# Optimization experiments

Measured on AMD Instinct MI355X. Metric: run time of the kernel, lower is better.

## Reference

```python
import jax, jax.numpy as jnp
import numpy as np

LN_EPS = 1e-12  # config.layer_norm_eps (BERT default)


def setup_inputs() -> dict:
    key = jax.random.key(0)
    k1, k2, k3, k4 = jax.random.split(key, 4)
    B, S, D_IN, D_OUT = 16, 512, 4096, 1024
    return {
        "hidden_states": jax.random.normal(k1, (B, S, D_IN), dtype=jnp.float32),
        "input_tensor": jax.random.normal(k2, (B, S, D_OUT), dtype=jnp.float32),
        "W": jax.random.normal(k3, (D_OUT, D_IN), dtype=jnp.float32) * 0.02,
        "b": jax.random.normal(k4, (D_OUT,), dtype=jnp.float32) * 0.02,
        "gamma": jnp.ones((D_OUT,), dtype=jnp.float32),
        "beta": jnp.zeros((D_OUT,), dtype=jnp.float32),
    }


def reference(hidden_states, input_tensor, W, b, gamma, beta):
    # mix_Linear 1-bit path (XNOR-Net style): binarize weights with per-row scale
    alpha = jnp.mean(jnp.abs(W), axis=1, keepdims=True)   # [D_OUT, 1]
    W_q = jnp.sign(W) * alpha                              # [D_OUT, D_IN]
    # dense GEMM: [B,S,D_IN] x [D_OUT,D_IN]^T -> [B,S,D_OUT]
    h = jnp.einsum("bsi,oi->bso", hidden_states, W_q) + b
    # dropout is identity in eval mode; residual add + LayerNorm
    x = h + input_tensor
    mu = jnp.mean(x, axis=-1, keepdims=True)
    var = jnp.mean(jnp.square(x - mu), axis=-1, keepdims=True)
    return gamma * (x - mu) * jax.lax.rsqrt(var + LN_EPS) + beta
```

## Files before the change

### kernel.cpp

```cpp
#include <hip/hip_runtime.h>

using u16    = unsigned short;
using short8 = __attribute__((ext_vector_type(8))) short;
using u16x8  = __attribute__((ext_vector_type(8))) u16;
using u16x4  = __attribute__((ext_vector_type(4))) u16;
using f32x4  = __attribute__((ext_vector_type(4))) float;

#define M_DIM 8192
#define N_DIM 1024
#define K_DIM 4096

typedef __attribute__((address_space(1))) void gvoid;
typedef __attribute__((address_space(3))) void svoid;
#define GLOAD_LDS16(g, s) \
  __builtin_amdgcn_global_load_lds((gvoid*)(void*)(g), (svoid*)(s), 16, 0, 0)

__device__ __forceinline__ u16 f2bf(float f) {
  unsigned u = __builtin_bit_cast(unsigned, f);
  u = (u + 0x7FFFu + ((u >> 16) & 1u)) >> 16;
  return (u16)u;
}

__global__ __launch_bounds__(256) void wprep_kernel(const float* __restrict__ W,
                                                    u16* __restrict__ Wsgn,
                                                    float* __restrict__ alpha) {
  const int row = blockIdx.x;
  const int t   = threadIdx.x;
  const float4* wr = (const float4*)(W + (size_t)row * K_DIM);
  float4 v[4];
  float s = 0.f;
#pragma unroll
  for (int j = 0; j < 4; ++j) {
    v[j] = wr[t + 256 * j];
    s += fabsf(v[j].x) + fabsf(v[j].y) + fabsf(v[j].z) + fabsf(v[j].w);
  }
#pragma unroll
  for (int off = 32; off > 0; off >>= 1) s += __shfl_down(s, off, 64);
  __shared__ float red[4];
  if ((t & 63) == 0) red[t >> 6] = s;
  __syncthreads();
  if (t == 0) alpha[row] = (red[0] + red[1] + red[2] + red[3]) * (1.0f / K_DIM);
  u16x4* dst = (u16x4*)(Wsgn + (size_t)row * K_DIM);
#pragma unroll
  for (int j = 0; j < 4; ++j) {
    u16x4 sg;
    sg[0] = v[j].x > 0.f ? 0x3F80 : (v[j].x < 0.f ? 0xBF80 : 0);
    sg[1] = v[j].y > 0.f ? 0x3F80 : (v[j].y < 0.f ? 0xBF80 : 0);
    sg[2] = v[j].z > 0.f ? 0x3F80 : (v[j].z < 0.f ? 0xBF80 : 0);
    sg[3] = v[j].w > 0.f ? 0x3F80 : (v[j].w < 0.f ? 0xBF80 : 0);
    dst[t + 256 * j] = sg;
  }
}

__global__ __launch_bounds__(256) void cast_kernel(const float* __restrict__ in,
                                                   u16* __restrict__ out) {
  const size_t i = ((size_t)blockIdx.x * 256 + threadIdx.x) * 8;
  float4 a = ((const float4*)(in + i))[0];
  float4 b = ((const float4*)(in + i))[1];
  u16x8 p;
  p[0] = f2bf(a.x); p[1] = f2bf(a.y); p[2] = f2bf(a.z); p[3] = f2bf(a.w);
  p[4] = f2bf(b.x); p[5] = f2bf(b.y); p[6] = f2bf(b.z); p[7] = f2bf(b.w);
  *(u16x8*)(out + i) = p;
}

template <bool PRE>
__global__ __launch_bounds__(256) void gemm_kernel(const void* __restrict__ Aopaque,
                                                   const u16* __restrict__ Bsgn,
                                                   const float* __restrict__ alpha,
                                                   const float* __restrict__ bias,
                                                   const float* __restrict__ resid,
                                                   float* __restrict__ out) {
  __shared__ u16 lA[128 * 64];
  __shared__ u16 lB[128 * 64];
  const int tid  = threadIdx.x;
  const int wave = tid >> 6;
  const int lane = tid & 63;
  const int quad = lane >> 4;
  const int l16  = lane & 15;
  const int wm   = (wave >> 1) * 64;
  const int wn   = (wave & 1) * 64;

  const int b    = blockIdx.x;
  const int xcd  = b & 7;
  const int l    = b >> 3;
  const size_t m0 = (size_t)(xcd * 8 + (l >> 3)) * 128;
  const size_t n0 = (size_t)(l & 7) * 128;

  f32x4 acc[4][4] = {};

  const int r8  = lane >> 3;
  const int kgs = ((lane & 7) ^ r8) * 8;
  const u16*   bsrc[4];
  const u16*   asrc16[4];
  u16*         bdst[4];
  u16*         adst[4];
#pragma unroll
  for (int j = 0; j < 4; ++j) {
    const int c = wave * 4 + j;
    bsrc[j] = Bsgn + (n0 + (size_t)c * 8 + r8) * K_DIM + kgs;
    bdst[j] = lB + c * 512;
    if constexpr (PRE)
      asrc16[j] = (const u16*)Aopaque + (m0 + (size_t)c * 8 + r8) * K_DIM + kgs;
    adst[j] = lA + c * 512;
  }

  for (int k0 = 0; k0 < K_DIM; k0 += 64) {
#pragma unroll
    for (int j = 0; j < 4; ++j) GLOAD_LDS16(bsrc[j] + k0, bdst[j]);
    if constexpr (PRE) {
#pragma unroll
      for (int j = 0; j < 4; ++j) GLOAD_LDS16(asrc16[j] + k0, adst[j]);
    } else {
      const float* A = (const float*)Aopaque;
      const int row = tid >> 1;
      const int h   = tid & 1;
#pragma unroll
      for (int g = 0; g < 4; ++g) {
        const int kg = h * 4 + g;
        const float4* src = (const float4*)(A + (m0 + row) * (size_t)K_DIM +
                                            k0 + kg * 8);
        float4 f0 = src[0], f1 = src[1];
        u16x8 p;
        p[0] = f2bf(f0.x); p[1] = f2bf(f0.y); p[2] = f2bf(f0.z); p[3] = f2bf(f0.w);
        p[4] = f2bf(f1.x); p[5] = f2bf(f1.y); p[6] = f2bf(f1.z); p[7] = f2bf(f1.w);
        *(u16x8*)(lA + row * 64 + ((kg ^ (row & 7)) * 8)) = p;
      }
    }
    asm volatile("s_waitcnt vmcnt(0)" ::: "memory");
    __syncthreads();

#pragma unroll
    for (int s = 0; s < 2; ++s) {
      short8 af[4], bf[4];
#pragma unroll
      for (int mt = 0; mt < 4; ++mt) {
        const int row = wm + mt * 16 + l16;
        af[mt] = *(const short8*)(lA + row * 64 + (((s * 4 + quad) ^ (row & 7)) * 8));
      }
#pragma unroll
      for (int nt = 0; nt < 4; ++nt) {
        const int col = wn + nt * 16 + l16;
        bf[nt] = *(const short8*)(lB + col * 64 + (((s * 4 + quad) ^ (col & 7)) * 8));
      }
#pragma unroll
      for (int mt = 0; mt < 4; ++mt)
#pragma unroll
        for (int nt = 0; nt < 4; ++nt)
          acc[mt][nt] = __builtin_amdgcn_mfma_f32_16x16x32_bf16(af[mt], bf[nt],
                                                                acc[mt][nt], 0, 0, 0);
    }
    __syncthreads();
  }

#pragma unroll
  for (int nt = 0; nt < 4; ++nt) {
    const size_t n  = n0 + wn + nt * 16 + l16;
    const float  al = alpha[n];
    const float  bi = bias[n];
#pragma unroll
    for (int mt = 0; mt < 4; ++mt) {
      const size_t mbase = m0 + wm + mt * 16 + quad * 4;
#pragma unroll
      for (int r = 0; r < 4; ++r) {
        const size_t mm = mbase + r;
        out[mm * N_DIM + n] = acc[mt][nt][r] * al + bi + resid[mm * N_DIM + n];
      }
    }
  }
}

__global__ __launch_bounds__(256) void ln_kernel(float* __restrict__ x,
                                                 const float* __restrict__ gamma,
                                                 const float* __restrict__ beta) {
  const size_t row = blockIdx.x;
  float4* xr = (float4*)(x + row * N_DIM);
  const int t = threadIdx.x;
  float4 v = xr[t];
  float s  = v.x + v.y + v.z + v.w;
  float sq = v.x * v.x + v.y * v.y + v.z * v.z + v.w * v.w;
#pragma unroll
  for (int off = 32; off > 0; off >>= 1) {
    s  += __shfl_down(s, off, 64);
    sq += __shfl_down(sq, off, 64);
  }
  __shared__ float rs[4], rq[4];
  if ((t & 63) == 0) { rs[t >> 6] = s; rq[t >> 6] = sq; }
  __syncthreads();
  s  = rs[0] + rs[1] + rs[2] + rs[3];
  sq = rq[0] + rq[1] + rq[2] + rq[3];
  const float mu  = s * (1.0f / N_DIM);
  float var = sq * (1.0f / N_DIM) - mu * mu;
  var = fmaxf(var, 0.0f);
  const float inv = rsqrtf(var + 1e-12f);
  const float4 g = ((const float4*)gamma)[t];
  const float4 b = ((const float4*)beta)[t];
  v.x = g.x * ((v.x - mu) * inv) + b.x;
  v.y = g.y * ((v.y - mu) * inv) + b.y;
  v.z = g.z * ((v.z - mu) * inv) + b.z;
  v.w = g.w * ((v.w - mu) * inv) + b.w;
  xr[t] = v;
}

extern "C" void kernel_launch(void* const* d_in, const int* in_sizes, int n_in,
                              void* d_out, int out_size, void* d_ws, size_t ws_size,
                              hipStream_t stream) {
  const float* hidden = (const float*)d_in[0];
  const float* resid  = (const float*)d_in[1];
  const float* W      = (const float*)d_in[2];
  const float* bias   = (const float*)d_in[3];
  const float* gamma  = (const float*)d_in[4];
  const float* beta   = (const float*)d_in[5];
  float* out = (float*)d_out;

  char* ws = (char*)d_ws;
  u16*   Wsgn  = (u16*)ws;
  float* alpha = (float*)(ws + 8ull * 1024 * 1024);
  u16*   Abf   = (u16*)(ws + 8ull * 1024 * 1024 + 4096);
  const size_t need_full = 8ull * 1024 * 1024 + 4096 + 64ull * 1024 * 1024;

  wprep_kernel<<<N_DIM, 256, 0, stream>>>(W, Wsgn, alpha);

  const int nblocks = (N_DIM / 128) * (M_DIM / 128);
  if (ws_size >= need_full) {
    cast_kernel<<<(M_DIM * (size_t)K_DIM) / (256 * 8), 256, 0, stream>>>(hidden, Abf);
    gemm_kernel<true><<<nblocks, 256, 0, stream>>>((const void*)Abf, Wsgn, alpha,
                                                   bias, resid, out);
  } else {
    gemm_kernel<false><<<nblocks, 256, 0, stream>>>((const void*)hidden, Wsgn, alpha,
                                                    bias, resid, out);
  }
  ln_kernel<<<M_DIM, 256, 0, stream>>>(out, gamma, beta);
}
```

Measured before the change: 330.9 us.

## Fuse fp32-to-bf16 cast of activations into GEMM via direct LDS fp32 staging

Removes the separate cast kernel and its bf16 workspace copy of the 8192x4096 activation matrix. The GEMM now streams fp32 activations straight into LDS with global_load_lds, using an XOR swizzle, and converts them to bf16 when building the MFMA fragments. This saves a full write and reread of the intermediate bf16 matrix. In exchange it doubles the A-tile LDS footprint and per-iteration global traffic, and adds conversion ALU work in the inner loop, where each A tile is converted by both N-side waves.

Measured after the change: 338.1 us. +2.2%, slower.

```diff
diff --git a/kernel.cpp b/kernel.cpp
--- a/kernel.cpp
+++ b/kernel.cpp
@@ -1,8 +1,8 @@
 #include <hip/hip_runtime.h>
+#include <hip/hip_bf16.h>
 
 using u16    = unsigned short;
 using short8 = __attribute__((ext_vector_type(8))) short;
-using u16x8  = __attribute__((ext_vector_type(8))) u16;
 using u16x4  = __attribute__((ext_vector_type(4))) u16;
 using f32x4  = __attribute__((ext_vector_type(4))) float;
 
@@ -14,12 +14,6 @@
 typedef __attribute__((address_space(3))) void svoid;
 #define GLOAD_LDS16(g, s) \
   __builtin_amdgcn_global_load_lds((gvoid*)(void*)(g), (svoid*)(s), 16, 0, 0)
-
-__device__ __forceinline__ u16 f2bf(float f) {
-  unsigned u = __builtin_bit_cast(unsigned, f);
-  u = (u + 0x7FFFu + ((u >> 16) & 1u)) >> 16;
-  return (u16)u;
-}
 
 __global__ __launch_bounds__(256) void wprep_kernel(const float* __restrict__ W,
                                                     u16* __restrict__ Wsgn,
@@ -52,26 +46,23 @@
   }
 }
 
-__global__ __launch_bounds__(256) void cast_kernel(const float* __restrict__ in,
-                                                   u16* __restrict__ out) {
-  const size_t i = ((size_t)blockIdx.x * 256 + threadIdx.x) * 8;
-  float4 a = ((const float4*)(in + i))[0];
-  float4 b = ((const float4*)(in + i))[1];
-  u16x8 p;
-  p[0] = f2bf(a.x); p[1] = f2bf(a.y); p[2] = f2bf(a.z); p[3] = f2bf(a.w);
-  p[4] = f2bf(b.x); p[5] = f2bf(b.y); p[6] = f2bf(b.z); p[7] = f2bf(b.w);
-  *(u16x8*)(out + i) = p;
-}
-
-template <bool PRE>
-__global__ __launch_bounds__(256) void gemm_kernel(const void* __restrict__ Aopaque,
+__device__ __forceinline__ short8 pack_bf16x8(f32x4 lo, f32x4 hi) {
+  union { short8 s; __hip_bfloat162 h[4]; } u;
+  u.h[0] = __float22bfloat162_rn(make_float2(lo[0], lo[1]));
+  u.h[1] = __float22bfloat162_rn(make_float2(lo[2], lo[3]));
+  u.h[2] = __float22bfloat162_rn(make_float2(hi[0], hi[1]));
+  u.h[3] = __float22bfloat162_rn(make_float2(hi[2], hi[3]));
+  return u.s;
+}
+
+__global__ __launch_bounds__(256) void gemm_kernel(const float* __restrict__ A,
                                                    const u16* __restrict__ Bsgn,
                                                    const float* __restrict__ alpha,
                                                    const float* __restrict__ bias,
                                                    const float* __restrict__ resid,
                                                    float* __restrict__ out) {
-  __shared__ u16 lA[128 * 64];
-  __shared__ u16 lB[128 * 64];
+  __shared__ float lA[128 * 64];
+  __shared__ u16   lB[128 * 64];
   const int tid  = threadIdx.x;
   const int wave = tid >> 6;
   const int lane = tid & 63;
@@ -89,58 +80,53 @@
   f32x4 acc[4][4] = {};
 
   const int r8  = lane >> 3;
-  const int kgs = ((lane & 7) ^ r8) * 8;
+  const int kgB = ((lane & 7) ^ r8) * 8;
+  const int r4  = lane >> 4;
+  const int gA  = lane & 15;
+
   const u16*   bsrc[4];
-  const u16*   asrc16[4];
   u16*         bdst[4];
-  u16*         adst[4];
+  const float* asrc[8];
+  float*       adst[8];
 #pragma unroll
   for (int j = 0; j < 4; ++j) {
     const int c = wave * 4 + j;
-    bsrc[j] = Bsgn + (n0 + (size_t)c * 8 + r8) * K_DIM + kgs;
+    bsrc[j] = Bsgn + (n0 + (size_t)c * 8 + r8) * K_DIM + kgB;
     bdst[j] = lB + c * 512;
-    if constexpr (PRE)
-      asrc16[j] = (const u16*)Aopaque + (m0 + (size_t)c * 8 + r8) * K_DIM + kgs;
-    adst[j] = lA + c * 512;
+  }
+#pragma unroll
+  for (int j = 0; j < 8; ++j) {
+    const int c   = wave * 8 + j;
+    const int row = c * 4 + r4;
+    asrc[j] = A + (m0 + row) * (size_t)K_DIM + (gA ^ (row & 7)) * 4;
+    adst[j] = lA + c * 256;
   }
 
   for (int k0 = 0; k0 < K_DIM; k0 += 64) {
 #pragma unroll
     for (int j = 0; j < 4; ++j) GLOAD_LDS16(bsrc[j] + k0, bdst[j]);
-    if constexpr (PRE) {
-#pragma unroll
-      for (int j = 0; j < 4; ++j) GLOAD_LDS16(asrc16[j] + k0, adst[j]);
-    } else {
-      const float* A = (const float*)Aopaque;
-      const int row = tid >> 1;
-      const int h   = tid & 1;
-#pragma unroll
-      for (int g = 0; g < 4; ++g) {
-        const int kg = h * 4 + g;
-        const float4* src = (const float4*)(A + (m0 + row) * (size_t)K_DIM +
-                                            k0 + kg * 8);
-        float4 f0 = src[0], f1 = src[1];
-        u16x8 p;
-        p[0] = f2bf(f0.x); p[1] = f2bf(f0.y); p[2] = f2bf(f0.z); p[3] = f2bf(f0.w);
-        p[4] = f2bf(f1.x); p[5] = f2bf(f1.y); p[6] = f2bf(f1.z); p[7] = f2bf(f1.w);
-        *(u16x8*)(lA + row * 64 + ((kg ^ (row & 7)) * 8)) = p;
-      }
-    }
+#pragma unroll
+    for (int j = 0; j < 8; ++j) GLOAD_LDS16(asrc[j] + k0, adst[j]);
     asm volatile("s_waitcnt vmcnt(0)" ::: "memory");
     __syncthreads();
 
 #pragma unroll
     for (int s = 0; s < 2; ++s) {
+      const int kq = s * 4 + quad;
       short8 af[4], bf[4];
 #pragma unroll
       for (int mt = 0; mt < 4; ++mt) {
         const int row = wm + mt * 16 + l16;
-        af[mt] = *(const short8*)(lA + row * 64 + (((s * 4 + quad) ^ (row & 7)) * 8));
+        const float* rp = lA + row * 64;
+        const int sl = (kq * 2) ^ (row & 7);
+        f32x4 lo = *(const f32x4*)(rp + sl * 4);
+        f32x4 hi = *(const f32x4*)(rp + (sl ^ 1) * 4);
+        af[mt] = pack_bf16x8(lo, hi);
       }
 #pragma unroll
       for (int nt = 0; nt < 4; ++nt) {
         const int col = wn + nt * 16 + l16;
-        bf[nt] = *(const short8*)(lB + col * 64 + (((s * 4 + quad) ^ (col & 7)) * 8));
+        bf[nt] = *(const short8*)(lB + col * 64 + ((kq ^ (col & 7)) * 8));
       }
 #pragma unroll
       for (int mt = 0; mt < 4; ++mt)
@@ -215,19 +201,11 @@
   char* ws = (char*)d_ws;
   u16*   Wsgn  = (u16*)ws;
   float* alpha = (float*)(ws + 8ull * 1024 * 1024);
-  u16*   Abf   = (u16*)(ws + 8ull * 1024 * 1024 + 4096);
-  const size_t need_full = 8ull * 1024 * 1024 + 4096 + 64ull * 1024 * 1024;
 
   wprep_kernel<<<N_DIM, 256, 0, stream>>>(W, Wsgn, alpha);
 
   const int nblocks = (N_DIM / 128) * (M_DIM / 128);
-  if (ws_size >= need_full) {
-    cast_kernel<<<(M_DIM * (size_t)K_DIM) / (256 * 8), 256, 0, stream>>>(hidden, Abf);
-    gemm_kernel<true><<<nblocks, 256, 0, stream>>>((const void*)Abf, Wsgn, alpha,
-                                                   bias, resid, out);
-  } else {
-    gemm_kernel<false><<<nblocks, 256, 0, stream>>>((const void*)hidden, Wsgn, alpha,
-                                                    bias, resid, out);
-  }
+  gemm_kernel<<<nblocks, 256, 0, stream>>>(hidden, Wsgn, alpha, bias, resid, out);
+
   ln_kernel<<<M_DIM, 256, 0, stream>>>(out, gamma, beta);
 }
```

## Double-buffer LDS tiles in the GEMM to overlap loads with MFMA

Applied to the files above, without the earlier changes.

The GEMM now uses two LDS buffers for the A and B tiles. It prefetches the next K-slice with global_load_lds into the alternate buffer while the MFMAs run on the current one. This removes the per-iteration vmcnt(0) wait and one of the two barriers per step, aiming to hide global-load latency behind compute. The cost is double the LDS per block, which may cut occupancy. The explicit vmcnt wait is also gone, so correctness depends on the compiler inserting waits for the LDS-DMA writes, which could conservatively serialize the prefetch.

New measurement: 350.3 us. 1.06x slower.

```diff
diff --git a/kernel.cpp b/kernel.cpp
--- a/kernel.cpp
+++ b/kernel.cpp
@@ -70,8 +70,8 @@
                                                    const float* __restrict__ bias,
                                                    const float* __restrict__ resid,
                                                    float* __restrict__ out) {
-  __shared__ u16 lA[128 * 64];
-  __shared__ u16 lB[128 * 64];
+  __shared__ u16 lA[2][128 * 64];
+  __shared__ u16 lB[2][128 * 64];
   const int tid  = threadIdx.x;
   const int wave = tid >> 6;
   const int lane = tid & 63;
@@ -90,67 +90,80 @@
 
   const int r8  = lane >> 3;
   const int kgs = ((lane & 7) ^ r8) * 8;
-  const u16*   bsrc[4];
-  const u16*   asrc16[4];
-  u16*         bdst[4];
-  u16*         adst[4];
+  const u16* bsrc[4];
+  const u16* asrc16[4];
+  int        coff[4];
 #pragma unroll
   for (int j = 0; j < 4; ++j) {
     const int c = wave * 4 + j;
     bsrc[j] = Bsgn + (n0 + (size_t)c * 8 + r8) * K_DIM + kgs;
-    bdst[j] = lB + c * 512;
     if constexpr (PRE)
       asrc16[j] = (const u16*)Aopaque + (m0 + (size_t)c * 8 + r8) * K_DIM + kgs;
-    adst[j] = lA + c * 512;
-  }
-
-  for (int k0 = 0; k0 < K_DIM; k0 += 64) {
-#pragma unroll
-    for (int j = 0; j < 4; ++j) GLOAD_LDS16(bsrc[j] + k0, bdst[j]);
-    if constexpr (PRE) {
-#pragma unroll
-      for (int j = 0; j < 4; ++j) GLOAD_LDS16(asrc16[j] + k0, adst[j]);
-    } else {
-      const float* A = (const float*)Aopaque;
-      const int row = tid >> 1;
-      const int h   = tid & 1;
-#pragma unroll
-      for (int g = 0; g < 4; ++g) {
-        const int kg = h * 4 + g;
-        const float4* src = (const float4*)(A + (m0 + row) * (size_t)K_DIM +
-                                            k0 + kg * 8);
-        float4 f0 = src[0], f1 = src[1];
-        u16x8 p;
-        p[0] = f2bf(f0.x); p[1] = f2bf(f0.y); p[2] = f2bf(f0.z); p[3] = f2bf(f0.w);
-        p[4] = f2bf(f1.x); p[5] = f2bf(f1.y); p[6] = f2bf(f1.z); p[7] = f2bf(f1.w);
-        *(u16x8*)(lA + row * 64 + ((kg ^ (row & 7)) * 8)) = p;
-      }
-    }
-    asm volatile("s_waitcnt vmcnt(0)" ::: "memory");
+    coff[j] = c * 512;
+  }
+
+#define STAGE(K0, BUF)                                                         \
+  do {                                                                         \
+    _Pragma("unroll")                                                          \
+    for (int j = 0; j < 4; ++j) GLOAD_LDS16(bsrc[j] + (K0), &lB[BUF][coff[j]]); \
+    if constexpr (PRE) {                                                       \
+      _Pragma("unroll")                                                        \
+      for (int j = 0; j < 4; ++j) GLOAD_LDS16(asrc16[j] + (K0), &lA[BUF][coff[j]]); \
+    } else {                                                                   \
+      const float* Af = (const float*)Aopaque;                                 \
+      const int row = tid >> 1;                                                \
+      const int h   = tid & 1;                                                 \
+      _Pragma("unroll")                                                        \
+      for (int g = 0; g < 4; ++g) {                                            \
+        const int kg = h * 4 + g;                                              \
+        const float4* src = (const float4*)(Af + (m0 + row) * (size_t)K_DIM +  \
+                                            (K0) + kg * 8);                    \
+        float4 f0 = src[0], f1 = src[1];                                       \
+        u16x8 p;                                                               \
+        p[0] = f2bf(f0.x); p[1] = f2bf(f0.y); p[2] = f2bf(f0.z); p[3] = f2bf(f0.w); \
+        p[4] = f2bf(f1.x); p[5] = f2bf(f1.y); p[6] = f2bf(f1.z); p[7] = f2bf(f1.w); \
+        *(u16x8*)(&lA[BUF][row * 64 + ((kg ^ (row & 7)) * 8)]) = p;            \
+      }                                                                        \
+    }                                                                          \
+  } while (0)
+
+#define COMPUTE(BUF)                                                           \
+  do {                                                                         \
+    _Pragma("unroll")                                                          \
+    for (int s = 0; s < 2; ++s) {                                              \
+      const int kq = s * 4 + quad;                                             \
+      short8 af[4], bf[4];                                                     \
+      _Pragma("unroll")                                                        \
+      for (int mt = 0; mt < 4; ++mt) {                                         \
+        const int row = wm + mt * 16 + l16;                                    \
+        af[mt] = *(const short8*)(&lA[BUF][row * 64 + ((kq ^ (row & 7)) * 8)]); \
+      }                                                                        \
+      _Pragma("unroll")                                                        \
+      for (int nt = 0; nt < 4; ++nt) {                                         \
+        const int col = wn + nt * 16 + l16;                                    \
+        bf[nt] = *(const short8*)(&lB[BUF][col * 64 + ((kq ^ (col & 7)) * 8)]); \
+      }                                                                        \
+      _Pragma("unroll")                                                        \
+      for (int mt = 0; mt < 4; ++mt)                                           \
+        _Pragma("unroll")                                                      \
+        for (int nt = 0; nt < 4; ++nt)                                         \
+          acc[mt][nt] = __builtin_amdgcn_mfma_f32_16x16x32_bf16(af[mt], bf[nt], \
+                                                                acc[mt][nt], 0, 0, 0); \
+    }                                                                          \
+  } while (0)
+
+  STAGE(0, 0);
+  __syncthreads();
+
+  int cur = 0;
+#pragma unroll 1
+  for (int k0 = 0; k0 < K_DIM - 64; k0 += 64) {
+    STAGE(k0 + 64, cur ^ 1);
+    COMPUTE(cur);
     __syncthreads();
-
-#pragma unroll
-    for (int s = 0; s < 2; ++s) {
-      short8 af[4], bf[4];
-#pragma unroll
-      for (int mt = 0; mt < 4; ++mt) {
-        const int row = wm + mt * 16 + l16;
-        af[mt] = *(const short8*)(lA + row * 64 + (((s * 4 + quad) ^ (row & 7)) * 8));
-      }
-#pragma unroll
-      for (int nt = 0; nt < 4; ++nt) {
-        const int col = wn + nt * 16 + l16;
-        bf[nt] = *(const short8*)(lB + col * 64 + (((s * 4 + quad) ^ (col & 7)) * 8));
-      }
-#pragma unroll
-      for (int mt = 0; mt < 4; ++mt)
-#pragma unroll
-        for (int nt = 0; nt < 4; ++nt)
-          acc[mt][nt] = __builtin_amdgcn_mfma_f32_16x16x32_bf16(af[mt], bf[nt],
-                                                                acc[mt][nt], 0, 0, 0);
-    }
-    __syncthreads();
-  }
+    cur ^= 1;
+  }
+  COMPUTE(cur);
 
 #pragma unroll
   for (int nt = 0; nt < 4; ++nt) {
@@ -167,6 +180,8 @@
       }
     }
   }
+#undef STAGE
+#undef COMPUTE
 }
 
 __global__ __launch_bounds__(256) void ln_kernel(float* __restrict__ x,
```
